# Performance work log

Hardware: AMD Instinct MI355X
Metric: run time of the kernel (lower is better)

## Reference

```python
import jax, jax.numpy as jnp
import numpy as np

K = 9          # neighbors = conv1d kernel = stride
OUT_CH = 64


def setup_inputs() -> dict:
    key = jax.random.key(0)
    k1, k2 = jax.random.split(key)
    x = jax.random.normal(k1, (8, 32, 56, 56), dtype=jnp.float32)
    W = jax.random.normal(k2, (OUT_CH, 32, K), dtype=jnp.float32) * 0.05  # conv1d weight (O,I,K), no bias
    return {"x": x, "W": W}


def reference(x, W):
    B, C, H, Wd = x.shape
    T = H * Wd
    xf = x.reshape(B, C, T)                                   # flatten spatial dims
    # cosine similarity matrix (F.normalize with eps=1e-12)
    nrm = jnp.sqrt(jnp.sum(xf * xf, axis=1, keepdims=True))
    xn = xf / jnp.maximum(nrm, 1e-12)
    sim = jnp.einsum('bct,bcs->bts', xn, xn)                  # [B,T,T]
    sim = jnp.clip(sim, -1.0, 1.0)
    sim = jnp.where(jnp.eye(T, dtype=bool)[None], 1.1, sim)   # self always top-1
    # top-K largest, then sort indices ascending (as in torch code)
    _, idx = jax.lax.top_k(sim, K)                            # [B,T,K]
    idx = jnp.sort(idx, axis=-1)
    # gather neighbor features: prime[b,c,t,k] = xf[b,c,idx[b,t,k]]
    prime = jax.vmap(lambda xb, ib: xb[:, ib])(xf, idx)       # [B,C,T,K]
    prime = prime.reshape(B, C, T * K)
    # conv1d kernel=K stride=K, no bias -> length T
    out = jax.lax.conv_general_dilated(
        prime, W, window_strides=(K,), padding='VALID',
        dimension_numbers=('NCH', 'OIH', 'NCH'))              # [B,OUT_CH,T]
    return out.reshape(B, OUT_CH, H, Wd)
```

## Files before the change

kernel.cpp:

```cpp
#include <hip/hip_runtime.h>
#include <stdint.h>
#include <math.h>

#define BB 8
#define CC 32
#define TT 3136
#define KK 9
#define OC 64

__global__ __launch_bounds__(256) void norm_kernel(
    const float* __restrict__ x, float* __restrict__ xfT, double* __restrict__ invn)
{
    int t = blockIdx.x * 256 + threadIdx.x;
    int b = blockIdx.y;
    if (t >= TT) return;
    const float* xp = x + (size_t)b * CC * TT + t;
    float v[CC];
    double ss = 0.0;
#pragma unroll
    for (int c = 0; c < CC; ++c) {
        v[c] = xp[(size_t)c * TT];
        ss = fma((double)v[c], (double)v[c], ss);
    }
    invn[(size_t)b * TT + t] = 1.0 / fmax(sqrt(ss), 1e-12);
    float* pf = xfT + ((size_t)b * TT + t) * CC;
#pragma unroll
    for (int c = 0; c < CC; c += 4)
        *(float4*)(pf + c) = make_float4(v[c], v[c+1], v[c+2], v[c+3]);
}

#define STILE 64
#define RPB   32

__global__ __launch_bounds__(256) void topk_kernel(
    const float* __restrict__ xfT, const double* __restrict__ invn,
    int* __restrict__ idxo)
{
    __shared__ double cols[STILE * 34];
    __shared__ double mval[256 * 8];
    __shared__ int    midx[256 * 8];

    int tid = threadIdx.x;
    int b   = blockIdx.y;
    int r   = tid >> 3;
    int q   = tid & 7;
    int t   = blockIdx.x * RPB + r;

    const float* rowp = xfT + ((size_t)b * TT + t) * CC;
    double rv[CC];
#pragma unroll
    for (int c = 0; c < CC; c += 4) {
        float4 f = *(const float4*)(rowp + c);
        rv[c] = (double)f.x; rv[c+1] = (double)f.y;
        rv[c+2] = (double)f.z; rv[c+3] = (double)f.w;
    }

    double val[8];
    int    ids[8];
#pragma unroll
    for (int j = 0; j < 8; ++j) { val[j] = -1.0e300; ids[j] = 0x7FFFFFFF; }

    int scol = tid >> 2;
    int part = tid & 3;

    for (int s0 = 0; s0 < TT; s0 += STILE) {
        __syncthreads();
        const float* gp = xfT + ((size_t)b * TT + (s0 + scol)) * CC + part * 8;
        float4 a0 = *(const float4*)(gp);
        float4 a1 = *(const float4*)(gp + 4);
        double* cd = &cols[scol * 34 + part * 8];
        cd[0] = (double)a0.x; cd[1] = (double)a0.y;
        cd[2] = (double)a0.z; cd[3] = (double)a0.w;
        cd[4] = (double)a1.x; cd[5] = (double)a1.y;
        cd[6] = (double)a1.z; cd[7] = (double)a1.w;
        if (part == 3) cols[scol * 34 + 32] = invn[(size_t)b * TT + (s0 + scol)];
        __syncthreads();

#pragma unroll
        for (int i = 0; i < STILE / 8; ++i) {
            int sl = i * 8 + q;
            int s  = s0 + sl;
            const double* cb = &cols[sl * 34];
            double acc = 0.0;
#pragma unroll
            for (int c = 0; c < CC; c += 2) {
                double2 cv = *(const double2*)(cb + c);
                acc = fma(rv[c],   cv.x, acc);
                acc = fma(rv[c+1], cv.y, acc);
            }
            double scr = acc * cb[32];
            if (s == t) continue;
            if (scr > val[7]) {
                val[7] = scr; ids[7] = s;
#pragma unroll
                for (int j = 7; j > 0; --j) {
                    if (val[j] > val[j-1]) {
                        double tv = val[j]; val[j] = val[j-1]; val[j-1] = tv;
                        int    ti = ids[j]; ids[j] = ids[j-1]; ids[j-1] = ti;
                    }
                }
            }
        }
    }

#pragma unroll
    for (int j = 0; j < 8; ++j) { mval[tid * 8 + j] = val[j]; midx[tid * 8 + j] = ids[j]; }
    __syncthreads();

    if (q == 0) {
        int p[8] = {0,0,0,0,0,0,0,0};
        int oi[9];
#pragma unroll
        for (int m = 0; m < 8; ++m) {
            double best = -1.0e301; int bi = 0x7FFFFFFF; int bq = 0;
#pragma unroll
            for (int qq = 0; qq < 8; ++qq) {
                if (p[qq] < 8) {
                    int base = (r * 8 + qq) * 8 + p[qq];
                    double v = mval[base]; int id = midx[base];
                    if (v > best || (v == best && id < bi)) { best = v; bi = id; bq = qq; }
                }
            }
            ++p[bq];
            oi[m] = bi;
        }
        oi[8] = t;
        for (int a = 1; a < 9; ++a) {
            int kv = oi[a]; int jj = a - 1;
            while (jj >= 0 && oi[jj] > kv) { oi[jj+1] = oi[jj]; --jj; }
            oi[jj+1] = kv;
        }
        int* op = idxo + ((size_t)b * TT + t) * KK;
#pragma unroll
        for (int m = 0; m < 9; ++m) op[m] = oi[m];
    }
}

__global__ __launch_bounds__(256) void gconv_kernel(
    const float* __restrict__ xfT, const int* __restrict__ idxi,
    const float* __restrict__ Wt, float* __restrict__ out)
{
    __shared__ float wl[288 * 65];
    __shared__ float ot[4][64 * 17];

    int tid = threadIdx.x;
    int b   = blockIdx.y;
    int t0  = blockIdx.x * 64;

    for (int f = tid; f < OC * 288; f += 256) {
        int o  = f / 288;
        int ck = f - o * 288;
        wl[ck * 65 + o] = Wt[f];
    }
    __syncthreads();

    int w    = tid >> 6;
    int lane = tid & 63;
    int tw0  = t0 + w * 16;

    for (int i = 0; i < 16; ++i) {
        int t = tw0 + i;
        const int* ip = idxi + ((size_t)b * TT + t) * KK;
        float acc = 0.f;
#pragma unroll
        for (int k = 0; k < KK; ++k) {
            int s = __builtin_amdgcn_readfirstlane(ip[k]);
            const float* col = xfT + ((size_t)b * TT + s) * CC;
#pragma unroll
            for (int c4 = 0; c4 < CC; c4 += 4) {
                float4 xv = *(const float4*)(col + c4);
                acc = fmaf(xv.x, wl[((c4+0)*9 + k)*65 + lane], acc);
                acc = fmaf(xv.y, wl[((c4+1)*9 + k)*65 + lane], acc);
                acc = fmaf(xv.z, wl[((c4+2)*9 + k)*65 + lane], acc);
                acc = fmaf(xv.w, wl[((c4+3)*9 + k)*65 + lane], acc);
            }
        }
        ot[w][lane * 17 + i] = acc;
    }
    __syncthreads();

    for (int j = 0; j < 16; ++j) {
        int fl = j * 64 + lane;
        int o  = fl >> 4;
        int ii = fl & 15;
        out[((size_t)b * OC + o) * TT + tw0 + ii] = ot[w][o * 17 + ii];
    }
}

extern "C" void kernel_launch(void* const* d_in, const int* in_sizes, int n_in,
                              void* d_out, int out_size, void* d_ws, size_t ws_size,
                              hipStream_t stream)
{
    const float* x  = (const float*)d_in[0];
    const float* Wt = (const float*)d_in[1];
    float* out = (float*)d_out;

    float*  xfT  = (float*)d_ws;
    double* invn = (double*)(xfT + (size_t)BB * TT * CC);
    int*    idw  = (int*)(invn + (size_t)BB * TT);

    dim3 g1((TT + 255) / 256, BB);
    norm_kernel<<<g1, 256, 0, stream>>>(x, xfT, invn);

    dim3 g2(TT / RPB, BB);
    topk_kernel<<<g2, 256, 0, stream>>>(xfT, invn, idw);

    dim3 g3(TT / 64, BB);
    gconv_kernel<<<g3, 256, 0, stream>>>(xfT, idw, Wt, out);
}
```

Before: 452.7 us.

## Screen top-k candidates in fp32 with pre-normalized rows, rescore finalists in fp64

The norm kernel now also writes a pre-normalized fp32 copy of the features. The top-k scan runs its similarity dot products in fp32 over 128-column tiles and keeps a 12-entry candidate list per thread. Each tile uses a wave-wide early exit and branchless insertion. The merged top-12 candidates are rescored in fp64 to pick the final 8, which removes most of the fp64 arithmetic. The risk is that fp32 rounding could push a true top-8 neighbor out of the 12-candidate margin.

```diff
diff --git a/kernel.cpp b/kernel.cpp
--- a/kernel.cpp
+++ b/kernel.cpp
@@ -8,8 +8,11 @@
 #define KK 9
 #define OC 64
 
+#define NEGINF (-3.0e38f)
+
 __global__ __launch_bounds__(256) void norm_kernel(
-    const float* __restrict__ x, float* __restrict__ xfT, double* __restrict__ invn)
+    const float* __restrict__ x, float* __restrict__ xnT,
+    float* __restrict__ xfT, double* __restrict__ invn)
 {
     int t = blockIdx.x * 256 + threadIdx.x;
     int b = blockIdx.y;
@@ -22,113 +25,183 @@
         v[c] = xp[(size_t)c * TT];
         ss = fma((double)v[c], (double)v[c], ss);
     }
-    invn[(size_t)b * TT + t] = 1.0 / fmax(sqrt(ss), 1e-12);
+    double inv = 1.0 / fmax(sqrt(ss), 1e-12);
+    invn[(size_t)b * TT + t] = inv;
+    float invf = (float)inv;
     float* pf = xfT + ((size_t)b * TT + t) * CC;
-#pragma unroll
-    for (int c = 0; c < CC; c += 4)
+    float* pn = xnT + ((size_t)b * TT + t) * CC;
+#pragma unroll
+    for (int c = 0; c < CC; c += 4) {
         *(float4*)(pf + c) = make_float4(v[c], v[c+1], v[c+2], v[c+3]);
-}
-
-#define STILE 64
-#define RPB   32
+        *(float4*)(pn + c) = make_float4(v[c]*invf, v[c+1]*invf, v[c+2]*invf, v[c+3]*invf);
+    }
+}
+
+__device__ __forceinline__ void insert12(float (&val)[12], int (&ids)[12],
+                                         float s, int idx)
+{
+#pragma unroll
+    for (int j = 11; j >= 1; --j) {
+        bool up   = s > val[j-1];
+        bool here = (s > val[j]) && !up;
+        val[j] = up ? val[j-1] : (here ? s   : val[j]);
+        ids[j] = up ? ids[j-1] : (here ? idx : ids[j]);
+    }
+    if (s > val[0]) { val[0] = s; ids[0] = idx; }
+}
+
+__device__ __forceinline__ void insert12_u64(uint64_t (&kv)[12], uint64_t k)
+{
+#pragma unroll
+    for (int j = 11; j >= 1; --j) {
+        bool up   = k > kv[j-1];
+        bool here = (k > kv[j]) && !up;
+        kv[j] = up ? kv[j-1] : (here ? k : kv[j]);
+    }
+    if (k > kv[0]) kv[0] = k;
+}
+
+template<int JN>
+__device__ __forceinline__ void scan_tile(
+    const float* __restrict__ cols, const float (&rv)[CC],
+    float (&val)[12], int (&ids)[12], int q, int t, int s0)
+{
+    float sc[JN];
+#pragma unroll
+    for (int j = 0; j < JN; ++j) sc[j] = 0.f;
+
+#pragma unroll
+    for (int c = 0; c < CC; c += 4) {
+        float rx = rv[c], ry = rv[c+1], rz = rv[c+2], rw = rv[c+3];
+#pragma unroll
+        for (int j = 0; j < JN; ++j) {
+            float4 cv = *(const float4*)(cols + (j*8 + q)*36 + c);
+            sc[j] = fmaf(rx, cv.x, sc[j]);
+            sc[j] = fmaf(ry, cv.y, sc[j]);
+            sc[j] = fmaf(rz, cv.z, sc[j]);
+            sc[j] = fmaf(rw, cv.w, sc[j]);
+        }
+    }
+#pragma unroll
+    for (int j = 0; j < JN; ++j)
+        if (s0 + j*8 + q == t) sc[j] = NEGINF;
+
+    for (int pass = 0; pass < JN; ++pass) {
+        float m = sc[0]; int am = 0;
+#pragma unroll
+        for (int j = 1; j < JN; ++j) {
+            bool g = sc[j] > m;
+            m  = g ? sc[j] : m;
+            am = g ? j : am;
+        }
+        bool want = m > val[11];
+        if (!__any(want)) break;
+        if (want) {
+            insert12(val, ids, m, s0 + am*8 + q);
+#pragma unroll
+            for (int j = 0; j < JN; ++j)
+                if (am == j) sc[j] = NEGINF;
+        }
+    }
+}
 
 __global__ __launch_bounds__(256) void topk_kernel(
-    const float* __restrict__ xfT, const double* __restrict__ invn,
-    int* __restrict__ idxo)
-{
-    __shared__ double cols[STILE * 34];
-    __shared__ double mval[256 * 8];
-    __shared__ int    midx[256 * 8];
+    const float* __restrict__ xnT, const float* __restrict__ xfT,
+    const double* __restrict__ invn, int* __restrict__ idxo)
+{
+    __shared__ uint64_t mbuf[32 * 97];
+    float* cols = (float*)mbuf;
 
     int tid = threadIdx.x;
     int b   = blockIdx.y;
     int r   = tid >> 3;
     int q   = tid & 7;
-    int t   = blockIdx.x * RPB + r;
-
-    const float* rowp = xfT + ((size_t)b * TT + t) * CC;
-    double rv[CC];
+    int t   = blockIdx.x * 32 + r;
+
+    const float* rowp = xnT + ((size_t)b * TT + t) * CC;
+    float rv[CC];
 #pragma unroll
     for (int c = 0; c < CC; c += 4) {
         float4 f = *(const float4*)(rowp + c);
-        rv[c] = (double)f.x; rv[c+1] = (double)f.y;
-        rv[c+2] = (double)f.z; rv[c+3] = (double)f.w;
-    }
-
-    double val[8];
-    int    ids[8];
-#pragma unroll
-    for (int j = 0; j < 8; ++j) { val[j] = -1.0e300; ids[j] = 0x7FFFFFFF; }
-
-    int scol = tid >> 2;
-    int part = tid & 3;
-
-    for (int s0 = 0; s0 < TT; s0 += STILE) {
+        rv[c] = f.x; rv[c+1] = f.y; rv[c+2] = f.z; rv[c+3] = f.w;
+    }
+
+    float val[12]; int ids[12];
+#pragma unroll
+    for (int j = 0; j < 12; ++j) { val[j] = NEGINF; ids[j] = 0x7FFFFFFF; }
+
+    for (int s0 = 0; s0 < TT; s0 += 128) {
+        int count = min(128, TT - s0);
         __syncthreads();
-        const float* gp = xfT + ((size_t)b * TT + (s0 + scol)) * CC + part * 8;
-        float4 a0 = *(const float4*)(gp);
-        float4 a1 = *(const float4*)(gp + 4);
-        double* cd = &cols[scol * 34 + part * 8];
-        cd[0] = (double)a0.x; cd[1] = (double)a0.y;
-        cd[2] = (double)a0.z; cd[3] = (double)a0.w;
-        cd[4] = (double)a1.x; cd[5] = (double)a1.y;
-        cd[6] = (double)a1.z; cd[7] = (double)a1.w;
-        if (part == 3) cols[scol * 34 + 32] = invn[(size_t)b * TT + (s0 + scol)];
+        for (int f = tid; f < count * 8; f += 256) {
+            int col = f >> 3, part = f & 7;
+            *(float4*)(cols + col*36 + part*4) =
+                *(const float4*)(xnT + ((size_t)b * TT + s0 + col) * CC + part*4);
+        }
         __syncthreads();
-
-#pragma unroll
-        for (int i = 0; i < STILE / 8; ++i) {
-            int sl = i * 8 + q;
-            int s  = s0 + sl;
-            const double* cb = &cols[sl * 34];
+        if (count == 128) scan_tile<16>(cols, rv, val, ids, q, t, s0);
+        else              scan_tile<8> (cols, rv, val, ids, q, t, s0);
+    }
+    __syncthreads();
+
+#pragma unroll
+    for (int j = 0; j < 12; ++j) {
+        uint32_t u = __float_as_uint(val[j]);
+        u = (u & 0x80000000u) ? ~u : (u | 0x80000000u);
+        mbuf[r*97 + q*12 + j] = ((uint64_t)u << 32) | (uint64_t)(~(uint32_t)ids[j]);
+    }
+    __syncthreads();
+
+    if (q == 0) {
+        uint64_t kv[12];
+#pragma unroll
+        for (int j = 0; j < 12; ++j) kv[j] = 0ull;
+        for (int i = 0; i < 96; ++i) {
+            uint64_t k = mbuf[r*97 + i];
+            if (k > kv[11]) insert12_u64(kv, k);
+        }
+
+        const float* rawp = xfT + ((size_t)b * TT + t) * CC;
+#pragma unroll
+        for (int c = 0; c < CC; c += 4) {
+            float4 f = *(const float4*)(rawp + c);
+            rv[c] = f.x; rv[c+1] = f.y; rv[c+2] = f.z; rv[c+3] = f.w;
+        }
+
+        double v8[8]; int i8[8];
+#pragma unroll
+        for (int j = 0; j < 8; ++j) { v8[j] = -1.0e300; i8[j] = 0x7FFFFFFF; }
+        for (int jc = 0; jc < 12; ++jc) {
+            int idx = (int)(~(uint32_t)kv[jc]);
+            const float* cp = xfT + ((size_t)b * TT + idx) * CC;
             double acc = 0.0;
 #pragma unroll
-            for (int c = 0; c < CC; c += 2) {
-                double2 cv = *(const double2*)(cb + c);
-                acc = fma(rv[c],   cv.x, acc);
-                acc = fma(rv[c+1], cv.y, acc);
+            for (int c = 0; c < CC; ++c)
+                acc = fma((double)rv[c], (double)cp[c], acc);
+            double scr = acc * invn[(size_t)b * TT + idx];
+
+            bool better7 = (scr > v8[7]) || (scr == v8[7] && idx < i8[7]);
+            if (better7) {
+#pragma unroll
+                for (int j = 7; j >= 1; --j) {
+                    bool up   = (scr > v8[j-1]) || (scr == v8[j-1] && idx < i8[j-1]);
+                    bool here = ((scr > v8[j]) || (scr == v8[j] && idx < i8[j])) && !up;
+                    v8[j] = up ? v8[j-1] : (here ? scr : v8[j]);
+                    i8[j] = up ? i8[j-1] : (here ? idx : i8[j]);
+                }
+                bool top = (scr > v8[0]) || (scr == v8[0] && idx < i8[0]);
+                if (top) { v8[0] = scr; i8[0] = idx; }
             }
-            double scr = acc * cb[32];
-            if (s == t) continue;
-            if (scr > val[7]) {
-                val[7] = scr; ids[7] = s;
-#pragma unroll
-                for (int j = 7; j > 0; --j) {
-                    if (val[j] > val[j-1]) {
-                        double tv = val[j]; val[j] = val[j-1]; val[j-1] = tv;
-                        int    ti = ids[j]; ids[j] = ids[j-1]; ids[j-1] = ti;
-                    }
-                }
-            }
-        }
-    }
-
-#pragma unroll
-    for (int j = 0; j < 8; ++j) { mval[tid * 8 + j] = val[j]; midx[tid * 8 + j] = ids[j]; }
-    __syncthreads();
-
-    if (q == 0) {
-        int p[8] = {0,0,0,0,0,0,0,0};
+        }
+
         int oi[9];
 #pragma unroll
-        for (int m = 0; m < 8; ++m) {
-            double best = -1.0e301; int bi = 0x7FFFFFFF; int bq = 0;
-#pragma unroll
-            for (int qq = 0; qq < 8; ++qq) {
-                if (p[qq] < 8) {
-                    int base = (r * 8 + qq) * 8 + p[qq];
-                    double v = mval[base]; int id = midx[base];
-                    if (v > best || (v == best && id < bi)) { best = v; bi = id; bq = qq; }
-                }
-            }
-            ++p[bq];
-            oi[m] = bi;
-        }
+        for (int j = 0; j < 8; ++j) oi[j] = i8[j];
         oi[8] = t;
         for (int a = 1; a < 9; ++a) {
-            int kv = oi[a]; int jj = a - 1;
-            while (jj >= 0 && oi[jj] > kv) { oi[jj+1] = oi[jj]; --jj; }
-            oi[jj+1] = kv;
+            int kvv = oi[a]; int jj = a - 1;
+            while (jj >= 0 && oi[jj] > kvv) { oi[jj+1] = oi[jj]; --jj; }
+            oi[jj+1] = kvv;
         }
         int* op = idxo + ((size_t)b * TT + t) * KK;
 #pragma unroll
@@ -195,15 +268,16 @@
     const float* Wt = (const float*)d_in[1];
     float* out = (float*)d_out;
 
-    float*  xfT  = (float*)d_ws;
+    float*  xnT  = (float*)d_ws;
+    float*  xfT  = xnT + (size_t)BB * TT * CC;
     double* invn = (double*)(xfT + (size_t)BB * TT * CC);
     int*    idw  = (int*)(invn + (size_t)BB * TT);
 
     dim3 g1((TT + 255) / 256, BB);
-    norm_kernel<<<g1, 256, 0, stream>>>(x, xfT, invn);
-
-    dim3 g2(TT / RPB, BB);
-    topk_kernel<<<g2, 256, 0, stream>>>(xfT, invn, idw);
+    norm_kernel<<<g1, 256, 0, stream>>>(x, xnT, xfT, invn);
+
+    dim3 g2(TT / 32, BB);
+    topk_kernel<<<g2, 256, 0, stream>>>(xnT, xfT, invn, idw);
 
     dim3 g3(TT / 64, BB);
     gconv_kernel<<<g3, 256, 0, stream>>>(xfT, idw, Wt, out);
```

Result: slower. 539.6 us (+19.2%).
